# Kernel optimization log

Hardware: AMD Instinct MI355X
Metric: run time of the kernel (lower is better)

The kernel has to match this reference:

```python
import jax, jax.numpy as jnp
import numpy as np

UNITS = 128
N_CLASSES = 10
N_FEAT = 3
R_ON = 0.05      # time-gate open ratio
ALPHA = 0.001    # leak during closed phase
LN_EPS = 1e-3    # keras LayerNormalization default epsilon


def _time_gate(t, tau, s):
    # t: [B], tau/s: [U] -> k: [B, U]
    phi = jnp.mod(t[:, None] - s, tau) / tau
    k = jnp.where(phi < 0.5 * R_ON, 2.0 * phi / R_ON,
        jnp.where(phi < R_ON, 2.0 - 2.0 * phi / R_ON, ALPHA * phi))
    return k


def _plstm_step(x, t, h, c, Wx, Wh, b, tau, s):
    z = x @ Wx + h @ Wh + b                      # [B, 4U]
    i, f, g, o = jnp.split(z, 4, axis=-1)
    c_hat = jax.nn.sigmoid(f) * c + jax.nn.sigmoid(i) * jnp.tanh(g)
    h_hat = jax.nn.sigmoid(o) * jnp.tanh(c_hat)
    k = _time_gate(t, tau, s)
    return k * h_hat + (1.0 - k) * h, k * c_hat + (1.0 - k) * c


def _layer_norm(x, gamma, beta):
    mu = jnp.mean(x, axis=-1, keepdims=True)
    var = jnp.mean(jnp.square(x - mu), axis=-1, keepdims=True)
    return gamma * (x - mu) * jax.lax.rsqrt(var + LN_EPS) + beta


def setup_inputs() -> dict:
    key = jax.random.key(0)
    ks = jax.random.split(key, 16)
    B, T, F, U, C = 256, 1000, N_FEAT, UNITS, N_CLASSES
    inputs = jax.random.normal(ks[0], (B, T, F), dtype=jnp.float32)
    # strictly increasing-ish observation times per sequence
    times = jnp.cumsum(jax.random.uniform(ks[1], (B, T), dtype=jnp.float32), axis=1)
    sc_in = 1.0 / np.sqrt(F)
    sc_h = 1.0 / np.sqrt(U)
    Wx0 = jax.random.normal(ks[2], (F, 4 * U), dtype=jnp.float32) * sc_in
    Wh0 = jax.random.normal(ks[3], (U, 4 * U), dtype=jnp.float32) * sc_h
    b0 = jnp.zeros((4 * U,), dtype=jnp.float32)
    tau0 = jnp.exp(jax.random.uniform(ks[4], (U,), minval=0.0, maxval=3.0, dtype=jnp.float32))
    s0 = jax.random.uniform(ks[5], (U,), dtype=jnp.float32) * tau0
    Wx1 = jax.random.normal(ks[6], (U, 4 * U), dtype=jnp.float32) * sc_h
    Wh1 = jax.random.normal(ks[7], (U, 4 * U), dtype=jnp.float32) * sc_h
    b1 = jnp.zeros((4 * U,), dtype=jnp.float32)
    tau1 = jnp.exp(jax.random.uniform(ks[8], (U,), minval=0.0, maxval=3.0, dtype=jnp.float32))
    s1 = jax.random.uniform(ks[9], (U,), dtype=jnp.float32) * tau1
    gamma = jnp.ones((U,), dtype=jnp.float32)
    beta = jnp.zeros((U,), dtype=jnp.float32)
    Wfc = jax.random.normal(ks[10], (U, C), dtype=jnp.float32) * sc_h
    bfc = jnp.zeros((C,), dtype=jnp.float32)
    return {"inputs": inputs, "times": times, "Wx0": Wx0, "Wh0": Wh0, "b0": b0,
            "tau0": tau0, "s0": s0, "Wx1": Wx1, "Wh1": Wh1, "b1": b1,
            "tau1": tau1, "s1": s1, "gamma": gamma, "beta": beta,
            "Wfc": Wfc, "bfc": bfc}


def reference(inputs, times, Wx0, Wh0, b0, tau0, s0, Wx1, Wh1, b1, tau1, s1,
              gamma, beta, Wfc, bfc):
    B, T, F = inputs.shape
    U = Wh0.shape[0]
    x_t = jnp.transpose(inputs, (1, 0, 2))   # [T, B, F]
    t_t = jnp.transpose(times, (1, 0))       # [T, B]

    def step(carry, xt):
        h0, c0, h1, c1 = carry
        x, t = xt
        h0, c0 = _plstm_step(x, t, h0, c0, Wx0, Wh0, b0, tau0, s0)
        hn = _layer_norm(h0, gamma, beta)
        h1, c1 = _plstm_step(hn, t, h1, c1, Wx1, Wh1, b1, tau1, s1)
        probs = jax.nn.softmax(h1 @ Wfc + bfc, axis=-1)
        return (h0, c0, h1, c1), probs

    zeros = jnp.zeros((B, U), dtype=inputs.dtype)
    init = (zeros, zeros, zeros, zeros)
    _, out = jax.lax.scan(step, init, (x_t, t_t))  # out: [T, B, C]
    return jnp.transpose(out, (1, 0, 2))           # [B, T, C]
```

## Files before the change

kernel.cpp:

```cpp
#include <hip/hip_runtime.h>
#include <math.h>

constexpr int U      = 128;
constexpr int G4     = 512;
constexpr int NCls   = 10;
constexpr int TSTEPS = 1000;
constexpr int BATCH  = 256;


__device__ __forceinline__ float sigm(float x) {
    return 1.0f / (1.0f + __expf(-x));
}

__device__ __forceinline__ float tgate(float t, float tau, float s) {
    float r = fmodf(t - s, tau);
    if (r < 0.0f) r += tau;
    const float phi = r / tau;
    return (phi < 0.025f) ? 40.0f * phi
         : (phi < 0.05f)  ? 2.0f - 40.0f * phi
         : 0.001f * phi;
}

__global__ __launch_bounds__(1024, 1) void plstm_fused(
    const float* __restrict__ inputs,
    const float* __restrict__ times,
    const float* __restrict__ Wx0,
    const float* __restrict__ Wh0,
    const float* __restrict__ b0,
    const float* __restrict__ tau0,
    const float* __restrict__ s0,
    const float* __restrict__ Wx1,
    const float* __restrict__ Wh1,
    const float* __restrict__ b1,
    const float* __restrict__ tau1,
    const float* __restrict__ s1,
    const float* __restrict__ gamma_,
    const float* __restrict__ beta_,
    const float* __restrict__ Wfc,
    const float* __restrict__ bfc,
    float* __restrict__ out)
{
    const int tid = threadIdx.x;
    const int h   = tid >> 9;
    const int j   = tid & 511;
    const int b   = blockIdx.x;

    __shared__ __align__(16) float wh0c[2 * 8 * 512 * 4];
    __shared__ __align__(16) float zp[2][G4];
    __shared__ __align__(16) float zq[2][G4];
    __shared__ __align__(16) float h0s[U];
    __shared__ __align__(16) float gh0s[U];
    __shared__ __align__(16) float h1s[U];
    __shared__ __align__(16) float wfcs[U * 11];
    __shared__ float bfcs[NCls];
    __shared__ float red[4];
    __shared__ float gms[U], bts[U];

    if (tid < U) { gms[tid] = gamma_[tid]; bts[tid] = beta_[tid];
                   h0s[tid] = 0.f; gh0s[tid] = 0.f; h1s[tid] = 0.f; }
    for (int i = tid; i < U * NCls; i += 1024) {
        const int u = i / NCls, c = i - u * NCls;
        wfcs[u * 11 + c] = Wfc[i];
    }
    if (tid < NCls) bfcs[tid] = bfc[tid];
    #pragma unroll 4
    for (int it = 0; it < 32; ++it) {
        const int cr = it * 2 + (tid >> 9);
        const int r  = ((cr >> 5) << 6) + (cr & 31);
        const float v = Wh0[r * G4 + j];
        const int hh = cr >> 5, u4 = (cr & 31) >> 2, s = cr & 3;
        wh0c[(((hh * 8 + u4) * 512) + j) * 4 + s] = v;
    }
    __syncthreads();

    const int ub = h * 64;
    float Pj = 0.0f, Qj = 0.0f;
    #pragma unroll 8
    for (int m = 0; m < 64; ++m) {
        const float w = Wx1[(ub + m) * G4 + j];
        Qj += gms[ub + m] * w;
        Pj += bts[ub + m] * w;
    }

    const float bj0  = b0[j];
    const float bj1  = b1[j];
    const float wx00 = Wx0[j];
    const float wx01 = Wx0[G4 + j];
    const float wx02 = Wx0[2 * G4 + j];
    float tau0r = 0.f, s0r = 0.f, tau1r = 0.f, s1r = 0.f, gr = 0.f;
    if (tid < U) {
        tau0r = tau0[tid]; s0r = s0[tid];
        tau1r = tau1[tid]; s1r = s1[tid];
        gr = gms[tid];
    }
    float c0r = 0.f, c1r = 0.f, h0r = 0.f, h1r = 0.f;

    const float* __restrict__ wh0p = Wh0 + (ub + 32) * G4 + j;
    const float* __restrict__ wx1p = Wx1 + ub * G4 + j;
    const float* __restrict__ wh1p = Wh1 + ub * G4 + j;
    const float4* __restrict__ wc4 =
        reinterpret_cast<const float4*>(wh0c) + (h * 8) * 512 + j;
    const float* __restrict__ xp = inputs + (size_t)b * TSTEPS * 3;
    const float* __restrict__ tp = times  + (size_t)b * TSTEPS;
    float*       __restrict__ op = out    + (size_t)b * TSTEPS * NCls;

    float xa0 = xp[0], xa1 = xp[1], xa2 = xp[2], tva = tp[0];

    __syncthreads();

    for (int t = 0; t < TSTEPS; ++t) {
        const float x0 = xa0, x1 = xa1, x2 = xa2, tv = tva;
        const int tn = (t + 1 < TSTEPS) ? t + 1 : t;
        xa0 = xp[tn*3+0]; xa1 = xp[tn*3+1]; xa2 = xp[tn*3+2]; tva = tp[tn];

        float a0, a1, a2, a3;
        if (h == 0) { a0 = bj0 + x0 * wx00; a1 = x1 * wx01; a2 = x2 * wx02; a3 = 0.f; }
        else        { a0 = 0.f; a1 = 0.f; a2 = 0.f; a3 = 0.f; }
        #pragma unroll
        for (int u4 = 0; u4 < 8; ++u4) {
            const float4 w4 = wc4[u4 * 512];
            const float4 h4 = *reinterpret_cast<const float4*>(&h0s[ub + 4 * u4]);
            a0 += h4.x * w4.x; a1 += h4.y * w4.y;
            a2 += h4.z * w4.z; a3 += h4.w * w4.w;
        }
        #pragma unroll
        for (int m = 0; m < 32; m += 4) {
            const float w0 = wh0p[(m + 0) * G4];
            const float w1 = wh0p[(m + 1) * G4];
            const float w2 = wh0p[(m + 2) * G4];
            const float w3 = wh0p[(m + 3) * G4];
            const float4 h4 = *reinterpret_cast<const float4*>(&h0s[ub + 32 + m]);
            a0 += h4.x * w0; a1 += h4.y * w1;
            a2 += h4.z * w2; a3 += h4.w * w3;
        }
        zp[h][j] = (a0 + a1) + (a2 + a3);
        __syncthreads();

        if (tid < U) {
            const float zi = zp[0][tid]       + zp[1][tid];
            const float zf = zp[0][tid + 128] + zp[1][tid + 128];
            const float zg = zp[0][tid + 256] + zp[1][tid + 256];
            const float zo = zp[0][tid + 384] + zp[1][tid + 384];
            const float ig = sigm(zi);
            const float fg = sigm(zf);
            const float gg = tanhf(zg);
            const float og = sigm(zo);
            const float ch = fg * c0r + ig * gg;
            const float hh = og * tanhf(ch);
            const float k  = tgate(tv, tau0r, s0r);
            const float hn = k * hh + (1.0f - k) * h0r;
            c0r = k * ch + (1.0f - k) * c0r;
            h0r = hn;
            h0s[tid]  = hn;
            gh0s[tid] = gr * hn;
            float ssum = hn, qsum = hn * hn;
            #pragma unroll
            for (int off = 1; off < 64; off <<= 1) {
                ssum += __shfl_xor(ssum, off);
                qsum += __shfl_xor(qsum, off);
            }
            if ((tid & 63) == 0) {
                red[(tid >> 6) * 2]     = ssum;
                red[(tid >> 6) * 2 + 1] = qsum;
            }
        }
        __syncthreads();

        const float mu   = (red[0] + red[2]) * (1.0f / 128.0f);
        const float msq  = (red[1] + red[3]) * (1.0f / 128.0f);
        const float rstd = rsqrtf(msq - mu * mu + 1e-3f);

        float ax0 = 0.f, ax1 = 0.f, ax2 = 0.f, ax3 = 0.f;
        float ah0 = 0.f, ah1 = 0.f, ah2 = 0.f, ah3 = 0.f;
        #pragma unroll 4
        for (int m = 0; m < 64; m += 4) {
            const float wxa = wx1p[(m + 0) * G4];
            const float wxb = wx1p[(m + 1) * G4];
            const float wxc = wx1p[(m + 2) * G4];
            const float wxd = wx1p[(m + 3) * G4];
            const float wha = wh1p[(m + 0) * G4];
            const float whb = wh1p[(m + 1) * G4];
            const float whc = wh1p[(m + 2) * G4];
            const float whd = wh1p[(m + 3) * G4];
            const float4 g4 = *reinterpret_cast<const float4*>(&gh0s[ub + m]);
            const float4 h4 = *reinterpret_cast<const float4*>(&h1s[ub + m]);
            ax0 += g4.x * wxa;  ah0 += h4.x * wha;
            ax1 += g4.y * wxb;  ah1 += h4.y * whb;
            ax2 += g4.z * wxc;  ah2 += h4.z * whc;
            ax3 += g4.w * wxd;  ah3 += h4.w * whd;
        }
        const float Swx = (ax0 + ax1) + (ax2 + ax3);
        const float Swh = (ah0 + ah1) + (ah2 + ah3);
        zq[h][j] = (h == 0 ? bj1 : 0.f) + Pj + rstd * Swx - (mu * rstd) * Qj + Swh;
        __syncthreads();

        if (tid < U) {
            const float zi = zq[0][tid]       + zq[1][tid];
            const float zf = zq[0][tid + 128] + zq[1][tid + 128];
            const float zg = zq[0][tid + 256] + zq[1][tid + 256];
            const float zo = zq[0][tid + 384] + zq[1][tid + 384];
            const float ig = sigm(zi);
            const float fg = sigm(zf);
            const float gg = tanhf(zg);
            const float og = sigm(zo);
            const float ch = fg * c1r + ig * gg;
            const float hh = og * tanhf(ch);
            const float k  = tgate(tv, tau1r, s1r);
            const float hn = k * hh + (1.0f - k) * h1r;
            c1r = k * ch + (1.0f - k) * c1r;
            h1r = hn;
            h1s[tid] = hn;
        }
        __syncthreads();

        if (tid < 64) {
            const float a  = h1s[tid];
            const float bv = h1s[tid + 64];
            float p[NCls];
            #pragma unroll
            for (int c = 0; c < NCls; ++c)
                p[c] = a * wfcs[tid * 11 + c] + bv * wfcs[(tid + 64) * 11 + c];
            #pragma unroll
            for (int off = 1; off < 64; off <<= 1) {
                #pragma unroll
                for (int c = 0; c < NCls; ++c) p[c] += __shfl_xor(p[c], off);
            }
            float m = -1e30f;
            #pragma unroll
            for (int c = 0; c < NCls; ++c) { p[c] += bfcs[c]; m = fmaxf(m, p[c]); }
            float ssum = 0.0f;
            #pragma unroll
            for (int c = 0; c < NCls; ++c) { p[c] = __expf(p[c] - m); ssum += p[c]; }
            const float inv = 1.0f / ssum;
            float pv = p[0];
            #pragma unroll
            for (int c = 1; c < NCls; ++c) if (tid == c) pv = p[c];
            if (tid < NCls) op[t * NCls + tid] = pv * inv;
        }
    }
}

extern "C" void kernel_launch(void* const* d_in, const int* in_sizes, int n_in,
                              void* d_out, int out_size, void* d_ws, size_t ws_size,
                              hipStream_t stream) {
    const float* inputs = (const float*)d_in[0];
    const float* times  = (const float*)d_in[1];
    const float* Wx0    = (const float*)d_in[2];
    const float* Wh0    = (const float*)d_in[3];
    const float* b0     = (const float*)d_in[4];
    const float* tau0   = (const float*)d_in[5];
    const float* s0     = (const float*)d_in[6];
    const float* Wx1    = (const float*)d_in[7];
    const float* Wh1    = (const float*)d_in[8];
    const float* b1     = (const float*)d_in[9];
    const float* tau1   = (const float*)d_in[10];
    const float* s1     = (const float*)d_in[11];
    const float* gamma_ = (const float*)d_in[12];
    const float* beta_  = (const float*)d_in[13];
    const float* Wfc    = (const float*)d_in[14];
    const float* bfc    = (const float*)d_in[15];
    float* out = (float*)d_out;

    dim3 grid(BATCH);
    dim3 block(1024);
    hipLaunchKernelGGL(plstm_fused, grid, block, 0, stream,
                       inputs, times, Wx0, Wh0, b0, tau0, s0,
                       Wx1, Wh1, b1, tau1, s1, gamma_, beta_, Wfc, bfc, out);
}
```

Measured before the change: 7.948 ms.

## Repartition recurrent matvecs so each thread computes four gate columns with float4 loads

Remaps the thread layout so each thread owns four adjacent gate columns and a slice of hidden-unit rows, reading weights as float4 for both layers. The first layer caches 48 rows of Wh0 in shared memory, split across 8 row groups. Bias and input projections move into the reduction phase, which sums the 8 partial results from shared memory. The intent is wider, more coalesced weight loads and more row-level parallelism, at the cost of a larger partial-sum buffer and an 8-way reduction done by only 128 threads.

```diff
diff --git a/kernel.cpp b/kernel.cpp
--- a/kernel.cpp
+++ b/kernel.cpp
@@ -6,6 +6,7 @@
 constexpr int NCls   = 10;
 constexpr int TSTEPS = 1000;
 constexpr int BATCH  = 256;
+constexpr int CROWS  = 48;
 
 
 __device__ __forceinline__ float sigm(float x) {
@@ -20,6 +21,13 @@
          : (phi < 0.05f)  ? 2.0f - 40.0f * phi
          : 0.001f * phi;
 }
+
+#define ROW4(WP, I, HB) { \
+    float4 w_; \
+    w_ = (WP)[((I)+0)*128]; ac.x += (HB).x*w_.x; ac.y += (HB).x*w_.y; ac.z += (HB).x*w_.z; ac.w += (HB).x*w_.w; \
+    w_ = (WP)[((I)+1)*128]; ac.x += (HB).y*w_.x; ac.y += (HB).y*w_.y; ac.z += (HB).y*w_.z; ac.w += (HB).y*w_.w; \
+    w_ = (WP)[((I)+2)*128]; ac.x += (HB).z*w_.x; ac.y += (HB).z*w_.y; ac.z += (HB).z*w_.z; ac.w += (HB).z*w_.w; \
+    w_ = (WP)[((I)+3)*128]; ac.x += (HB).w*w_.x; ac.y += (HB).w*w_.y; ac.z += (HB).w*w_.z; ac.w += (HB).w*w_.w; }
 
 __global__ __launch_bounds__(1024, 1) void plstm_fused(
     const float* __restrict__ inputs,
@@ -41,52 +49,49 @@
     float* __restrict__ out)
 {
     const int tid = threadIdx.x;
-    const int h   = tid >> 9;
-    const int j   = tid & 511;
+    const int c4  = tid & 127;
+    const int g   = tid >> 7;
     const int b   = blockIdx.x;
 
-    __shared__ __align__(16) float wh0c[2 * 8 * 512 * 4];
-    __shared__ __align__(16) float zp[2][G4];
-    __shared__ __align__(16) float zq[2][G4];
+    __shared__ __align__(16) float wh0c[CROWS * G4];
+    __shared__ __align__(16) float zu[8 * G4];
     __shared__ __align__(16) float h0s[U];
-    __shared__ __align__(16) float gh0s[U];
-    __shared__ __align__(16) float h1s[U];
+    __shared__ __align__(16) float ghu[2 * U];
+    __shared__ __align__(16) float b0s[G4], b1s[G4], Ps[G4], Qs[G4];
+    __shared__ __align__(16) float wx0s[3 * G4];
     __shared__ __align__(16) float wfcs[U * 11];
     __shared__ float bfcs[NCls];
     __shared__ float red[4];
     __shared__ float gms[U], bts[U];
 
     if (tid < U) { gms[tid] = gamma_[tid]; bts[tid] = beta_[tid];
-                   h0s[tid] = 0.f; gh0s[tid] = 0.f; h1s[tid] = 0.f; }
+                   h0s[tid] = 0.f; ghu[tid] = 0.f; ghu[U + tid] = 0.f; }
+    {
+        float4* dst = reinterpret_cast<float4*>(wh0c);
+        const float4* src = reinterpret_cast<const float4*>(Wh0);
+        #pragma unroll
+        for (int i = 0; i < 6; ++i) dst[tid + i * 1024] = src[tid + i * 1024];
+    }
+    if (tid < G4) { b0s[tid] = b0[tid]; b1s[tid] = b1[tid]; }
+    for (int i = tid; i < 3 * G4; i += 1024) wx0s[i] = Wx0[i];
     for (int i = tid; i < U * NCls; i += 1024) {
         const int u = i / NCls, c = i - u * NCls;
         wfcs[u * 11 + c] = Wfc[i];
     }
     if (tid < NCls) bfcs[tid] = bfc[tid];
-    #pragma unroll 4
-    for (int it = 0; it < 32; ++it) {
-        const int cr = it * 2 + (tid >> 9);
-        const int r  = ((cr >> 5) << 6) + (cr & 31);
-        const float v = Wh0[r * G4 + j];
-        const int hh = cr >> 5, u4 = (cr & 31) >> 2, s = cr & 3;
-        wh0c[(((hh * 8 + u4) * 512) + j) * 4 + s] = v;
-    }
     __syncthreads();
 
-    const int ub = h * 64;
-    float Pj = 0.0f, Qj = 0.0f;
-    #pragma unroll 8
-    for (int m = 0; m < 64; ++m) {
-        const float w = Wx1[(ub + m) * G4 + j];
-        Qj += gms[ub + m] * w;
-        Pj += bts[ub + m] * w;
-    }
-
-    const float bj0  = b0[j];
-    const float bj1  = b1[j];
-    const float wx00 = Wx0[j];
-    const float wx01 = Wx0[G4 + j];
-    const float wx02 = Wx0[2 * G4 + j];
+    if (tid < G4) {
+        float P = 0.f, Q = 0.f;
+        #pragma unroll 8
+        for (int u = 0; u < U; ++u) {
+            const float w = Wx1[u * G4 + tid];
+            Q += gms[u] * w;
+            P += bts[u] * w;
+        }
+        Ps[tid] = P; Qs[tid] = Q;
+    }
+
     float tau0r = 0.f, s0r = 0.f, tau1r = 0.f, s1r = 0.f, gr = 0.f;
     if (tid < U) {
         tau0r = tau0[tid]; s0r = s0[tid];
@@ -95,11 +100,6 @@
     }
     float c0r = 0.f, c1r = 0.f, h0r = 0.f, h1r = 0.f;
 
-    const float* __restrict__ wh0p = Wh0 + (ub + 32) * G4 + j;
-    const float* __restrict__ wx1p = Wx1 + ub * G4 + j;
-    const float* __restrict__ wh1p = Wh1 + ub * G4 + j;
-    const float4* __restrict__ wc4 =
-        reinterpret_cast<const float4*>(wh0c) + (h * 8) * 512 + j;
     const float* __restrict__ xp = inputs + (size_t)b * TSTEPS * 3;
     const float* __restrict__ tp = times  + (size_t)b * TSTEPS;
     float*       __restrict__ op = out    + (size_t)b * TSTEPS * NCls;
@@ -113,46 +113,51 @@
         const int tn = (t + 1 < TSTEPS) ? t + 1 : t;
         xa0 = xp[tn*3+0]; xa1 = xp[tn*3+1]; xa2 = xp[tn*3+2]; tva = tp[tn];
 
-        float a0, a1, a2, a3;
-        if (h == 0) { a0 = bj0 + x0 * wx00; a1 = x1 * wx01; a2 = x2 * wx02; a3 = 0.f; }
-        else        { a0 = 0.f; a1 = 0.f; a2 = 0.f; a3 = 0.f; }
-        #pragma unroll
-        for (int u4 = 0; u4 < 8; ++u4) {
-            const float4 w4 = wc4[u4 * 512];
-            const float4 h4 = *reinterpret_cast<const float4*>(&h0s[ub + 4 * u4]);
-            a0 += h4.x * w4.x; a1 += h4.y * w4.y;
-            a2 += h4.z * w4.z; a3 += h4.w * w4.w;
-        }
-        #pragma unroll
-        for (int m = 0; m < 32; m += 4) {
-            const float w0 = wh0p[(m + 0) * G4];
-            const float w1 = wh0p[(m + 1) * G4];
-            const float w2 = wh0p[(m + 2) * G4];
-            const float w3 = wh0p[(m + 3) * G4];
-            const float4 h4 = *reinterpret_cast<const float4*>(&h0s[ub + 32 + m]);
-            a0 += h4.x * w0; a1 += h4.y * w1;
-            a2 += h4.z * w2; a3 += h4.w * w3;
-        }
-        zp[h][j] = (a0 + a1) + (a2 + a3);
+        {
+            float4 ac = make_float4(0.f, 0.f, 0.f, 0.f);
+            const int r0 = g * 16;
+            if (g < 3) {
+                const float4* wp = reinterpret_cast<const float4*>(wh0c) + r0 * 128 + c4;
+                #pragma unroll 2
+                for (int i = 0; i < 16; i += 4) {
+                    const float4 hb = *reinterpret_cast<const float4*>(&h0s[r0 + i]);
+                    ROW4(wp, i, hb);
+                }
+            } else {
+                const float4* wp = reinterpret_cast<const float4*>(Wh0) + r0 * 128 + c4;
+                #pragma unroll 2
+                for (int i = 0; i < 16; i += 4) {
+                    const float4 hb = *reinterpret_cast<const float4*>(&h0s[r0 + i]);
+                    ROW4(wp, i, hb);
+                }
+            }
+            *reinterpret_cast<float4*>(&zu[g * G4 + 4 * c4]) = ac;
+        }
         __syncthreads();
 
         if (tid < U) {
-            const float zi = zp[0][tid]       + zp[1][tid];
-            const float zf = zp[0][tid + 128] + zp[1][tid + 128];
-            const float zg = zp[0][tid + 256] + zp[1][tid + 256];
-            const float zo = zp[0][tid + 384] + zp[1][tid + 384];
-            const float ig = sigm(zi);
-            const float fg = sigm(zf);
-            const float gg = tanhf(zg);
-            const float og = sigm(zo);
+            const int u = tid;
+            float z[4];
+            #pragma unroll
+            for (int q = 0; q < 4; ++q) {
+                const int c = u + q * 128;
+                float s = b0s[c] + x0 * wx0s[c] + x1 * wx0s[G4 + c] + x2 * wx0s[2 * G4 + c];
+                #pragma unroll
+                for (int gg = 0; gg < 8; ++gg) s += zu[gg * G4 + c];
+                z[q] = s;
+            }
+            const float ig = sigm(z[0]);
+            const float fg = sigm(z[1]);
+            const float gg = tanhf(z[2]);
+            const float og = sigm(z[3]);
             const float ch = fg * c0r + ig * gg;
             const float hh = og * tanhf(ch);
             const float k  = tgate(tv, tau0r, s0r);
             const float hn = k * hh + (1.0f - k) * h0r;
             c0r = k * ch + (1.0f - k) * c0r;
             h0r = hn;
-            h0s[tid]  = hn;
-            gh0s[tid] = gr * hn;
+            h0s[u] = hn;
+            ghu[u] = gr * hn;
             float ssum = hn, qsum = hn * hn;
             #pragma unroll
             for (int off = 1; off < 64; off <<= 1) {
@@ -166,56 +171,54 @@
         }
         __syncthreads();
 
-        const float mu   = (red[0] + red[2]) * (1.0f / 128.0f);
-        const float msq  = (red[1] + red[3]) * (1.0f / 128.0f);
-        const float rstd = rsqrtf(msq - mu * mu + 1e-3f);
-
-        float ax0 = 0.f, ax1 = 0.f, ax2 = 0.f, ax3 = 0.f;
-        float ah0 = 0.f, ah1 = 0.f, ah2 = 0.f, ah3 = 0.f;
-        #pragma unroll 4
-        for (int m = 0; m < 64; m += 4) {
-            const float wxa = wx1p[(m + 0) * G4];
-            const float wxb = wx1p[(m + 1) * G4];
-            const float wxc = wx1p[(m + 2) * G4];
-            const float wxd = wx1p[(m + 3) * G4];
-            const float wha = wh1p[(m + 0) * G4];
-            const float whb = wh1p[(m + 1) * G4];
-            const float whc = wh1p[(m + 2) * G4];
-            const float whd = wh1p[(m + 3) * G4];
-            const float4 g4 = *reinterpret_cast<const float4*>(&gh0s[ub + m]);
-            const float4 h4 = *reinterpret_cast<const float4*>(&h1s[ub + m]);
-            ax0 += g4.x * wxa;  ah0 += h4.x * wha;
-            ax1 += g4.y * wxb;  ah1 += h4.y * whb;
-            ax2 += g4.z * wxc;  ah2 += h4.z * whc;
-            ax3 += g4.w * wxd;  ah3 += h4.w * whd;
-        }
-        const float Swx = (ax0 + ax1) + (ax2 + ax3);
-        const float Swh = (ah0 + ah1) + (ah2 + ah3);
-        zq[h][j] = (h == 0 ? bj1 : 0.f) + Pj + rstd * Swx - (mu * rstd) * Qj + Swh;
+        {
+            const int half = tid >> 9;
+            const int rg   = (tid >> 7) & 3;
+            const int r0   = rg * 32;
+            const float* __restrict__ Wm = half ? Wh1 : Wx1;
+            const float* hvp = ghu + half * U + r0;
+            const float4* wp = reinterpret_cast<const float4*>(Wm) + r0 * 128 + c4;
+            float4 ac = make_float4(0.f, 0.f, 0.f, 0.f);
+            #pragma unroll 2
+            for (int i = 0; i < 32; i += 4) {
+                const float4 hb = *reinterpret_cast<const float4*>(&hvp[i]);
+                ROW4(wp, i, hb);
+            }
+            *reinterpret_cast<float4*>(&zu[(half * 4 + rg) * G4 + 4 * c4]) = ac;
+        }
         __syncthreads();
 
         if (tid < U) {
-            const float zi = zq[0][tid]       + zq[1][tid];
-            const float zf = zq[0][tid + 128] + zq[1][tid + 128];
-            const float zg = zq[0][tid + 256] + zq[1][tid + 256];
-            const float zo = zq[0][tid + 384] + zq[1][tid + 384];
-            const float ig = sigm(zi);
-            const float fg = sigm(zf);
-            const float gg = tanhf(zg);
-            const float og = sigm(zo);
+            const float mu    = (red[0] + red[2]) * (1.0f / 128.0f);
+            const float msq   = (red[1] + red[3]) * (1.0f / 128.0f);
+            const float rstd  = rsqrtf(msq - mu * mu + 1e-3f);
+            const float murstd = mu * rstd;
+            const int u = tid;
+            float z[4];
+            #pragma unroll
+            for (int q = 0; q < 4; ++q) {
+                const int c = u + q * 128;
+                const float sx = (zu[0*G4+c] + zu[1*G4+c]) + (zu[2*G4+c] + zu[3*G4+c]);
+                const float sh = (zu[4*G4+c] + zu[5*G4+c]) + (zu[6*G4+c] + zu[7*G4+c]);
+                z[q] = b1s[c] + Ps[c] + rstd * sx - murstd * Qs[c] + sh;
+            }
+            const float ig = sigm(z[0]);
+            const float fg = sigm(z[1]);
+            const float gg = tanhf(z[2]);
+            const float og = sigm(z[3]);
             const float ch = fg * c1r + ig * gg;
             const float hh = og * tanhf(ch);
             const float k  = tgate(tv, tau1r, s1r);
             const float hn = k * hh + (1.0f - k) * h1r;
             c1r = k * ch + (1.0f - k) * c1r;
             h1r = hn;
-            h1s[tid] = hn;
+            ghu[U + u] = hn;
         }
         __syncthreads();
 
         if (tid < 64) {
-            const float a  = h1s[tid];
-            const float bv = h1s[tid + 64];
+            const float a  = ghu[U + tid];
+            const float bv = ghu[U + tid + 64];
             float p[NCls];
             #pragma unroll
             for (int c = 0; c < NCls; ++c)
```

After: 7.087 ms. 1.12x faster.
